# Performance work log

Hardware: AMD Instinct MI355X
Metric: run time of the kernel (lower is better)

## Reference

```python
import jax, jax.numpy as jnp
import numpy as np

RADIUS = 8
EPS = 1e-4


def window_sum(x, rh, rw):
    # sliding-window sum with edge-truncated windows, via cumsum+slice+concat
    ch = jnp.cumsum(x, axis=2)
    wh = 2 * rh + 1
    top = ch[..., rh:wh, :]
    midh = ch[..., wh:, :] - ch[..., :-wh, :]
    bot = ch[..., -1:, :] - ch[..., -wh:-rh - 1, :]
    out = jnp.concatenate([top, midh, bot], axis=2)
    cw = jnp.cumsum(out, axis=3)
    ww = 2 * rw + 1
    left = cw[..., rw:ww]
    midw = cw[..., ww:] - cw[..., :-ww]
    right = cw[..., -1:] - cw[..., -ww:-rw - 1]
    return jnp.concatenate([left, midw, right], axis=3)


def box_mean(x, r):
    # normalized box filter: window sum / per-pixel valid count
    return window_sum(x, r, r) / window_sum(jnp.ones_like(x), r, r)


def setup_inputs() -> dict:
    key = jax.random.key(0)
    k1, k2, k3 = jax.random.split(key, 3)
    p_lr = jax.random.uniform(k1, (8, 3, 256, 256), dtype=jnp.float32)
    I_lr = jax.random.uniform(k2, (8, 3, 256, 256), dtype=jnp.float32)
    I_hr = jax.random.uniform(k3, (8, 3, 1024, 1024), dtype=jnp.float32)
    return {"p_lr": p_lr, "I_lr": I_lr, "I_hr": I_hr}


def reference(p_lr, I_lr, I_hr):
    r = RADIUS
    mean_I = box_mean(I_lr, r)
    mean_p = box_mean(p_lr, r)
    cov_Ip = box_mean(I_lr * p_lr, r) - mean_I * mean_p
    var_I = box_mean(I_lr * I_lr, r) - mean_I ** 2
    A_lr = cov_Ip / (var_I + EPS)
    B_lr = mean_p - A_lr * mean_I
    N, C = I_hr.shape[0], I_hr.shape[1]
    H, W = I_hr.shape[2], I_hr.shape[3]
    # bilinear, half-pixel centers == torch align_corners=False
    A_hr = jax.image.resize(A_lr, (N, C, H, W), method="linear")
    B_hr = jax.image.resize(B_lr, (N, C, H, W), method="linear")
    return A_hr * I_hr + B_hr
```

## Files before the change

### kernel.cpp

```cpp
#include <hip/hip_runtime.h>

#define RADIUS 8
#define LR 256
#define HRES 1024
#define NC 24
#define GF_EPS 1e-4f
#define FSTRIP 8

typedef float f4 __attribute__((ext_vector_type(4)));

__global__ __launch_bounds__(256) void kF(const float* __restrict__ p,
                                          const float* __restrict__ I,
                                          float* __restrict__ A, float* __restrict__ B) {
    __shared__ float vI[2][LR], vp[2][LR], vIp[2][LR], vII[2][LR];
    const int x     = threadIdx.x;
    const int img   = blockIdx.x >> 5;
    const int strip = blockIdx.x & 31;
    const int y0    = strip * FSTRIP;
    const int ib    = img * LR * LR;
    const float* Ii = I + ib;
    const float* pi = p + ib;

    float sI = 0.f, sp_ = 0.f, sIp = 0.f, sII = 0.f;
    #pragma unroll 1
    for (int yy = y0 - RADIUS; yy <= y0 + RADIUS; ++yy) {
        if (yy >= 0 && yy < LR) {
            const float vi = Ii[yy * LR + x];
            const float vq = pi[yy * LR + x];
            sI  += vi;
            sp_ += vq;
            sIp += vi * vq;
            sII += vi * vi;
        }
    }
    const int cntx = min(x + RADIUS, LR - 1) - max(x - RADIUS, 0) + 1;

    #pragma unroll 2
    for (int k = 0; k < FSTRIP; ++k) {
        const int y   = y0 + k;
        const int buf = k & 1;
        vI [buf][x] = sI;
        vp [buf][x] = sp_;
        vIp[buf][x] = sIp;
        vII[buf][x] = sII;
        __syncthreads();

        const int yadd = y + RADIUS + 1;
        const int ysub = y - RADIUS;
        float aI = 0.f, aq = 0.f, rI = 0.f, rq = 0.f;
        if (yadd < LR) { aI = Ii[yadd * LR + x]; aq = pi[yadd * LR + x]; }
        if (ysub >= 0) { rI = Ii[ysub * LR + x]; rq = pi[ysub * LR + x]; }

        float hI = 0.f, hp = 0.f, hIp = 0.f, hII = 0.f;
        #pragma unroll
        for (int t = -RADIUS; t <= RADIUS; ++t) {
            const int   xt = x + t;
            const int   xx = min(max(xt, 0), LR - 1);
            const float m  = ((unsigned)xt < (unsigned)LR) ? 1.f : 0.f;
            hI  = fmaf(m, vI [buf][xx], hI);
            hp  = fmaf(m, vp [buf][xx], hp);
            hIp = fmaf(m, vIp[buf][xx], hIp);
            hII = fmaf(m, vII[buf][xx], hII);
        }

        const int   cnty = min(y + RADIUS, LR - 1) - max(y - RADIUS, 0) + 1;
        const float inv  = 1.0f / (float)(cntx * cnty);
        const float mI   = hI * inv;
        const float mp   = hp * inv;
        const float cov  = hIp * inv - mI * mp;
        const float var  = hII * inv - mI * mI;
        const float a    = cov / (var + GF_EPS);
        const float bb   = mp - a * mI;
        const int   idx  = ib + y * LR + x;
        A[idx] = a;
        B[idx] = bb;

        sI  += aI - rI;
        sp_ += aq - rq;
        sIp += fmaf(aI, aq, -rI * rq);
        sII += fmaf(aI, aI, -rI * rI);
    }
}

__global__ __launch_bounds__(256) void kR(const float* __restrict__ A, const float* __restrict__ B,
                                          const float* __restrict__ Ihr, float* __restrict__ out) {
    __shared__ float av[8][LR];
    __shared__ float bv[8][LR];

    const int blk = blockIdx.x;
    const int img = blk >> 7;
    const int k2  = blk & 127;
    const int k   = k2 << 1;
    const int tx  = threadIdx.x;

    const float* Ai = A + img * LR * LR;
    const float* Bi = B + img * LR * LR;
    const int rm = max(k - 1, 0);
    const int rp = min(k + 2, LR - 1);

    const float aU = Ai[rm * LR + tx];
    const float a0 = Ai[k * LR + tx];
    const float a1 = Ai[(k + 1) * LR + tx];
    const float aD = Ai[rp * LR + tx];
    const float bU = Bi[rm * LR + tx];
    const float b0 = Bi[k * LR + tx];
    const float b1 = Bi[(k + 1) * LR + tx];
    const float bD = Bi[rp * LR + tx];

    av[0][tx] = aU + 0.625f * (a0 - aU);
    av[1][tx] = aU + 0.875f * (a0 - aU);
    av[2][tx] = a0 + 0.125f * (a1 - a0);
    av[3][tx] = a0 + 0.375f * (a1 - a0);
    av[4][tx] = a0 + 0.625f * (a1 - a0);
    av[5][tx] = a0 + 0.875f * (a1 - a0);
    av[6][tx] = a1 + 0.125f * (aD - a1);
    av[7][tx] = a1 + 0.375f * (aD - a1);
    bv[0][tx] = bU + 0.625f * (b0 - bU);
    bv[1][tx] = bU + 0.875f * (b0 - bU);
    bv[2][tx] = b0 + 0.125f * (b1 - b0);
    bv[3][tx] = b0 + 0.375f * (b1 - b0);
    bv[4][tx] = b0 + 0.625f * (b1 - b0);
    bv[5][tx] = b0 + 0.875f * (b1 - b0);
    bv[6][tx] = b1 + 0.125f * (bD - b1);
    bv[7][tx] = b1 + 0.375f * (bD - b1);
    __syncthreads();

    const long long base = ((long long)img << 20) + ((long long)k << 12) + (tx << 2);

    f4 ih[8];
    #pragma unroll
    for (int r = 0; r < 8; ++r)
        ih[r] = __builtin_nontemporal_load((const f4*)(Ihr + base + ((long long)r << 10)));

    const int cm1 = max(tx - 1, 0);
    const int cp1 = min(tx + 1, LR - 1);

    #pragma unroll
    for (int r = 0; r < 8; ++r) {
        const float am = av[r][cm1], ac = av[r][tx], ap = av[r][cp1];
        const float bm = bv[r][cm1], bc = bv[r][tx], bp = bv[r][cp1];
        float p0, p1, q0, q1;
        if (tx == 0) { p0 = ac; p1 = ac; q0 = bc; q1 = bc; }
        else {
            p0 = am + 0.625f * (ac - am);
            p1 = am + 0.875f * (ac - am);
            q0 = bm + 0.625f * (bc - bm);
            q1 = bm + 0.875f * (bc - bm);
        }
        const float p2 = ac + 0.125f * (ap - ac);
        const float p3 = ac + 0.375f * (ap - ac);
        const float q2 = bc + 0.125f * (bp - bc);
        const float q3 = bc + 0.375f * (bp - bc);

        f4 res;
        res.x = p0 * ih[r].x + q0;
        res.y = p1 * ih[r].y + q1;
        res.z = p2 * ih[r].z + q2;
        res.w = p3 * ih[r].w + q3;
        __builtin_nontemporal_store(res, (f4*)(out + base + ((long long)r << 10)));
    }
}

extern "C" void kernel_launch(void* const* d_in, const int* in_sizes, int n_in,
                              void* d_out, int out_size, void* d_ws, size_t ws_size,
                              hipStream_t stream) {
    const float* p_lr = (const float*)d_in[0];
    const float* I_lr = (const float*)d_in[1];
    const float* I_hr = (const float*)d_in[2];
    float* out = (float*)d_out;
    float* ws  = (float*)d_ws;

    const int S = NC * LR * LR;
    float* A = ws + 0 * (size_t)S;
    float* B = ws + 1 * (size_t)S;

    kF<<<NC * (LR / FSTRIP), 256, 0, stream>>>(p_lr, I_lr, A, B);
    kR<<<NC * 128, 256, 0, stream>>>(A, B, I_hr, out);
}
```

Measured before the change: 200.3 us.

## Fuse box-filter coefficient computation into the upsample kernel

Merges the low-res guided-filter coefficient kernel into the bilinear-upsample kernel, so each block recomputes the four low-res A/B rows it needs straight from I_lr and p_lr. This removes the A/B workspace round trip through global memory and one kernel launch. In exchange each low-res row is computed about twice, every block runs a 17-row vertical prefix loop, and the shared arrays are reused as column-sum buffers under an occupancy hint of 4 blocks per SM. The high-res loads are issued first so they can overlap the box-filter arithmetic.

```diff
diff --git a/kernel.cpp b/kernel.cpp
--- a/kernel.cpp
+++ b/kernel.cpp
@@ -2,88 +2,15 @@
 
 #define RADIUS 8
 #define LR 256
-#define HRES 1024
 #define NC 24
 #define GF_EPS 1e-4f
-#define FSTRIP 8
 
 typedef float f4 __attribute__((ext_vector_type(4)));
 
-__global__ __launch_bounds__(256) void kF(const float* __restrict__ p,
-                                          const float* __restrict__ I,
-                                          float* __restrict__ A, float* __restrict__ B) {
-    __shared__ float vI[2][LR], vp[2][LR], vIp[2][LR], vII[2][LR];
-    const int x     = threadIdx.x;
-    const int img   = blockIdx.x >> 5;
-    const int strip = blockIdx.x & 31;
-    const int y0    = strip * FSTRIP;
-    const int ib    = img * LR * LR;
-    const float* Ii = I + ib;
-    const float* pi = p + ib;
-
-    float sI = 0.f, sp_ = 0.f, sIp = 0.f, sII = 0.f;
-    #pragma unroll 1
-    for (int yy = y0 - RADIUS; yy <= y0 + RADIUS; ++yy) {
-        if (yy >= 0 && yy < LR) {
-            const float vi = Ii[yy * LR + x];
-            const float vq = pi[yy * LR + x];
-            sI  += vi;
-            sp_ += vq;
-            sIp += vi * vq;
-            sII += vi * vi;
-        }
-    }
-    const int cntx = min(x + RADIUS, LR - 1) - max(x - RADIUS, 0) + 1;
-
-    #pragma unroll 2
-    for (int k = 0; k < FSTRIP; ++k) {
-        const int y   = y0 + k;
-        const int buf = k & 1;
-        vI [buf][x] = sI;
-        vp [buf][x] = sp_;
-        vIp[buf][x] = sIp;
-        vII[buf][x] = sII;
-        __syncthreads();
-
-        const int yadd = y + RADIUS + 1;
-        const int ysub = y - RADIUS;
-        float aI = 0.f, aq = 0.f, rI = 0.f, rq = 0.f;
-        if (yadd < LR) { aI = Ii[yadd * LR + x]; aq = pi[yadd * LR + x]; }
-        if (ysub >= 0) { rI = Ii[ysub * LR + x]; rq = pi[ysub * LR + x]; }
-
-        float hI = 0.f, hp = 0.f, hIp = 0.f, hII = 0.f;
-        #pragma unroll
-        for (int t = -RADIUS; t <= RADIUS; ++t) {
-            const int   xt = x + t;
-            const int   xx = min(max(xt, 0), LR - 1);
-            const float m  = ((unsigned)xt < (unsigned)LR) ? 1.f : 0.f;
-            hI  = fmaf(m, vI [buf][xx], hI);
-            hp  = fmaf(m, vp [buf][xx], hp);
-            hIp = fmaf(m, vIp[buf][xx], hIp);
-            hII = fmaf(m, vII[buf][xx], hII);
-        }
-
-        const int   cnty = min(y + RADIUS, LR - 1) - max(y - RADIUS, 0) + 1;
-        const float inv  = 1.0f / (float)(cntx * cnty);
-        const float mI   = hI * inv;
-        const float mp   = hp * inv;
-        const float cov  = hIp * inv - mI * mp;
-        const float var  = hII * inv - mI * mI;
-        const float a    = cov / (var + GF_EPS);
-        const float bb   = mp - a * mI;
-        const int   idx  = ib + y * LR + x;
-        A[idx] = a;
-        B[idx] = bb;
-
-        sI  += aI - rI;
-        sp_ += aq - rq;
-        sIp += fmaf(aI, aq, -rI * rq);
-        sII += fmaf(aI, aI, -rI * rI);
-    }
-}
-
-__global__ __launch_bounds__(256) void kR(const float* __restrict__ A, const float* __restrict__ B,
-                                          const float* __restrict__ Ihr, float* __restrict__ out) {
+__global__ __launch_bounds__(256, 4) void kG(const float* __restrict__ p,
+                                             const float* __restrict__ I,
+                                             const float* __restrict__ Ihr,
+                                             float* __restrict__ out) {
     __shared__ float av[8][LR];
     __shared__ float bv[8][LR];
 
@@ -92,45 +19,91 @@
     const int k2  = blk & 127;
     const int k   = k2 << 1;
     const int tx  = threadIdx.x;
-
-    const float* Ai = A + img * LR * LR;
-    const float* Bi = B + img * LR * LR;
-    const int rm = max(k - 1, 0);
-    const int rp = min(k + 2, LR - 1);
-
-    const float aU = Ai[rm * LR + tx];
-    const float a0 = Ai[k * LR + tx];
-    const float a1 = Ai[(k + 1) * LR + tx];
-    const float aD = Ai[rp * LR + tx];
-    const float bU = Bi[rm * LR + tx];
-    const float b0 = Bi[k * LR + tx];
-    const float b1 = Bi[(k + 1) * LR + tx];
-    const float bD = Bi[rp * LR + tx];
-
-    av[0][tx] = aU + 0.625f * (a0 - aU);
-    av[1][tx] = aU + 0.875f * (a0 - aU);
-    av[2][tx] = a0 + 0.125f * (a1 - a0);
-    av[3][tx] = a0 + 0.375f * (a1 - a0);
-    av[4][tx] = a0 + 0.625f * (a1 - a0);
-    av[5][tx] = a0 + 0.875f * (a1 - a0);
-    av[6][tx] = a1 + 0.125f * (aD - a1);
-    av[7][tx] = a1 + 0.375f * (aD - a1);
-    bv[0][tx] = bU + 0.625f * (b0 - bU);
-    bv[1][tx] = bU + 0.875f * (b0 - bU);
-    bv[2][tx] = b0 + 0.125f * (b1 - b0);
-    bv[3][tx] = b0 + 0.375f * (b1 - b0);
-    bv[4][tx] = b0 + 0.625f * (b1 - b0);
-    bv[5][tx] = b0 + 0.875f * (b1 - b0);
-    bv[6][tx] = b1 + 0.125f * (bD - b1);
-    bv[7][tx] = b1 + 0.375f * (bD - b1);
-    __syncthreads();
+    const int ib  = img * LR * LR;
+    const float* Ii = I + ib;
+    const float* pi = p + ib;
 
     const long long base = ((long long)img << 20) + ((long long)k << 12) + (tx << 2);
-
     f4 ih[8];
     #pragma unroll
     for (int r = 0; r < 8; ++r)
         ih[r] = __builtin_nontemporal_load((const f4*)(Ihr + base + ((long long)r << 10)));
+
+    const int r0 = max(k - 1, 0);
+    float sI = 0.f, sp_ = 0.f, sIp = 0.f, sII = 0.f;
+    #pragma unroll 1
+    for (int yy = r0 - RADIUS; yy <= r0 + RADIUS; ++yy) {
+        if (yy >= 0 && yy < LR) {
+            const float vi = Ii[yy * LR + tx];
+            const float vq = pi[yy * LR + tx];
+            sI += vi; sp_ += vq; sIp += vi * vq; sII += vi * vi;
+        }
+    }
+    const int cntx = min(tx + RADIUS, LR - 1) - max(tx - RADIUS, 0) + 1;
+
+    float a_[4], b_[4];
+    int yprev = r0;
+    #pragma unroll
+    for (int j = 0; j < 4; ++j) {
+        const int y = min(max(k - 1 + j, 0), LR - 1);
+        if (y != yprev) {
+            const int yadd = y + RADIUS;
+            const int ysub = yprev - RADIUS;
+            if (yadd < LR) {
+                const float aI = Ii[yadd * LR + tx], aq = pi[yadd * LR + tx];
+                sI += aI; sp_ += aq; sIp += aI * aq; sII += aI * aI;
+            }
+            if (ysub >= 0) {
+                const float rI = Ii[ysub * LR + tx], rq = pi[ysub * LR + tx];
+                sI -= rI; sp_ -= rq; sIp -= rI * rq; sII -= rI * rI;
+            }
+        }
+        yprev = y;
+        const int buf = j & 1;
+        av[0 + buf][tx] = sI;
+        av[2 + buf][tx] = sp_;
+        av[4 + buf][tx] = sIp;
+        av[6 + buf][tx] = sII;
+        __syncthreads();
+        float hI = 0.f, hp = 0.f, hIp = 0.f, hII = 0.f;
+        #pragma unroll
+        for (int t = -RADIUS; t <= RADIUS; ++t) {
+            const int   xt = tx + t;
+            const int   xx = min(max(xt, 0), LR - 1);
+            const float m  = ((unsigned)xt < (unsigned)LR) ? 1.f : 0.f;
+            hI  = fmaf(m, av[0 + buf][xx], hI);
+            hp  = fmaf(m, av[2 + buf][xx], hp);
+            hIp = fmaf(m, av[4 + buf][xx], hIp);
+            hII = fmaf(m, av[6 + buf][xx], hII);
+        }
+        const int   cnty = min(y + RADIUS, LR - 1) - max(y - RADIUS, 0) + 1;
+        const float inv  = 1.0f / (float)(cntx * cnty);
+        const float mI   = hI * inv;
+        const float mp   = hp * inv;
+        const float cov  = hIp * inv - mI * mp;
+        const float var  = hII * inv - mI * mI;
+        a_[j] = cov / (var + GF_EPS);
+        b_[j] = mp - a_[j] * mI;
+    }
+    __syncthreads();
+
+    av[0][tx] = a_[0] + 0.625f * (a_[1] - a_[0]);
+    av[1][tx] = a_[0] + 0.875f * (a_[1] - a_[0]);
+    av[2][tx] = a_[1] + 0.125f * (a_[2] - a_[1]);
+    av[3][tx] = a_[1] + 0.375f * (a_[2] - a_[1]);
+    av[4][tx] = a_[1] + 0.625f * (a_[2] - a_[1]);
+    av[5][tx] = a_[1] + 0.875f * (a_[2] - a_[1]);
+    av[6][tx] = a_[2] + 0.125f * (a_[3] - a_[2]);
+    av[7][tx] = a_[2] + 0.375f * (a_[3] - a_[2]);
+    bv[0][tx] = b_[0] + 0.625f * (b_[1] - b_[0]);
+    bv[1][tx] = b_[0] + 0.875f * (b_[1] - b_[0]);
+    bv[2][tx] = b_[1] + 0.125f * (b_[2] - b_[1]);
+    bv[3][tx] = b_[1] + 0.375f * (b_[2] - b_[1]);
+    bv[4][tx] = b_[1] + 0.625f * (b_[2] - b_[1]);
+    bv[5][tx] = b_[1] + 0.875f * (b_[2] - b_[1]);
+    bv[6][tx] = b_[2] + 0.125f * (b_[3] - b_[2]);
+    bv[7][tx] = b_[2] + 0.375f * (b_[3] - b_[2]);
+    __syncthreads();
 
     const int cm1 = max(tx - 1, 0);
     const int cp1 = min(tx + 1, LR - 1);
@@ -168,12 +141,7 @@
     const float* I_lr = (const float*)d_in[1];
     const float* I_hr = (const float*)d_in[2];
     float* out = (float*)d_out;
-    float* ws  = (float*)d_ws;
+    (void)d_ws; (void)ws_size;
 
-    const int S = NC * LR * LR;
-    float* A = ws + 0 * (size_t)S;
-    float* B = ws + 1 * (size_t)S;
-
-    kF<<<NC * (LR / FSTRIP), 256, 0, stream>>>(p_lr, I_lr, A, B);
-    kR<<<NC * 128, 256, 0, stream>>>(A, B, I_hr, out);
+    kG<<<NC * 128, 256, 0, stream>>>(p_lr, I_lr, I_hr, out);
 }
```

Result: slower. 362.8 us (+81.1%).

## Batch strip vertical sums in shared memory and swizzle block-to-XCD mapping

Applied to the files above, without the earlier changes.

kF now writes all eight rows of vertical window sums into a larger shared array and then synchronizes once, replacing the per-row barrier and double buffer. Both kernels remap blockIdx so that consecutive work units land on the same XCD, assuming round-robin dispatch across 8 XCDs, to improve L2 locality. The cost is more shared memory per block (32KB), which may reduce occupancy in kF.

```diff
diff --git a/kernel.cpp b/kernel.cpp
--- a/kernel.cpp
+++ b/kernel.cpp
@@ -12,10 +12,11 @@
 __global__ __launch_bounds__(256) void kF(const float* __restrict__ p,
                                           const float* __restrict__ I,
                                           float* __restrict__ A, float* __restrict__ B) {
-    __shared__ float vI[2][LR], vp[2][LR], vIp[2][LR], vII[2][LR];
+    __shared__ float s[FSTRIP][4][LR];
+    const int swz   = ((blockIdx.x & 7) * 96) + (blockIdx.x >> 3);
     const int x     = threadIdx.x;
-    const int img   = blockIdx.x >> 5;
-    const int strip = blockIdx.x & 31;
+    const int img   = swz >> 5;
+    const int strip = swz & 31;
     const int y0    = strip * FSTRIP;
     const int ib    = img * LR * LR;
     const float* Ii = I + ib;
@@ -33,36 +34,42 @@
             sII += vi * vi;
         }
     }
-    const int cntx = min(x + RADIUS, LR - 1) - max(x - RADIUS, 0) + 1;
 
-    #pragma unroll 2
+    #pragma unroll
     for (int k = 0; k < FSTRIP; ++k) {
-        const int y   = y0 + k;
-        const int buf = k & 1;
-        vI [buf][x] = sI;
-        vp [buf][x] = sp_;
-        vIp[buf][x] = sIp;
-        vII[buf][x] = sII;
-        __syncthreads();
-
+        s[k][0][x] = sI;
+        s[k][1][x] = sp_;
+        s[k][2][x] = sIp;
+        s[k][3][x] = sII;
+        const int y    = y0 + k;
         const int yadd = y + RADIUS + 1;
         const int ysub = y - RADIUS;
-        float aI = 0.f, aq = 0.f, rI = 0.f, rq = 0.f;
-        if (yadd < LR) { aI = Ii[yadd * LR + x]; aq = pi[yadd * LR + x]; }
-        if (ysub >= 0) { rI = Ii[ysub * LR + x]; rq = pi[ysub * LR + x]; }
+        if (yadd < LR) {
+            const float aI = Ii[yadd * LR + x], aq = pi[yadd * LR + x];
+            sI += aI; sp_ += aq; sIp += aI * aq; sII += aI * aI;
+        }
+        if (ysub >= 0) {
+            const float rI = Ii[ysub * LR + x], rq = pi[ysub * LR + x];
+            sI -= rI; sp_ -= rq; sIp -= rI * rq; sII -= rI * rI;
+        }
+    }
+    __syncthreads();
 
+    const int cntx = min(x + RADIUS, LR - 1) - max(x - RADIUS, 0) + 1;
+    #pragma unroll
+    for (int k = 0; k < FSTRIP; ++k) {
         float hI = 0.f, hp = 0.f, hIp = 0.f, hII = 0.f;
         #pragma unroll
         for (int t = -RADIUS; t <= RADIUS; ++t) {
             const int   xt = x + t;
             const int   xx = min(max(xt, 0), LR - 1);
             const float m  = ((unsigned)xt < (unsigned)LR) ? 1.f : 0.f;
-            hI  = fmaf(m, vI [buf][xx], hI);
-            hp  = fmaf(m, vp [buf][xx], hp);
-            hIp = fmaf(m, vIp[buf][xx], hIp);
-            hII = fmaf(m, vII[buf][xx], hII);
+            hI  = fmaf(m, s[k][0][xx], hI);
+            hp  = fmaf(m, s[k][1][xx], hp);
+            hIp = fmaf(m, s[k][2][xx], hIp);
+            hII = fmaf(m, s[k][3][xx], hII);
         }
-
+        const int   y    = y0 + k;
         const int   cnty = min(y + RADIUS, LR - 1) - max(y - RADIUS, 0) + 1;
         const float inv  = 1.0f / (float)(cntx * cnty);
         const float mI   = hI * inv;
@@ -74,11 +81,6 @@
         const int   idx  = ib + y * LR + x;
         A[idx] = a;
         B[idx] = bb;
-
-        sI  += aI - rI;
-        sp_ += aq - rq;
-        sIp += fmaf(aI, aq, -rI * rq);
-        sII += fmaf(aI, aI, -rI * rI);
     }
 }
 
@@ -87,9 +89,9 @@
     __shared__ float av[8][LR];
     __shared__ float bv[8][LR];
 
-    const int blk = blockIdx.x;
-    const int img = blk >> 7;
-    const int k2  = blk & 127;
+    const int swz = ((blockIdx.x & 7) * 384) + (blockIdx.x >> 3);
+    const int img = swz >> 7;
+    const int k2  = swz & 127;
     const int k   = k2 << 1;
     const int tx  = threadIdx.x;
 
```

Result: slower. 206.0 us (+2.8%).
